# Optimization experiments

Measured on AMD Instinct MI355X. Metric: run time of the kernel, lower is better.

The kernel has to match this reference:

```python
import jax, jax.numpy as jnp
import numpy as np

NEG = 0.01
NEG2 = 0.2
EPS = 1e-5
K = 10            # args.nk // 2
B, N, NZ = 8, 2048, 128


def lrelu(x, s):
    return jnp.where(x >= 0, x, s * x)


def conv1(x, W, b):  # 1x1 Conv1d: x [B,C,N], W [O,C]
    return jnp.einsum('bcn,oc->bon', x, W) + b[None, :, None]


def conv2(x, W, b):  # 1x1 Conv2d: x [B,C,N,K], W [O,C]
    return jnp.einsum('bcnk,oc->bonk', x, W) + b[None, :, None, None]


def bn2d(x, g, b):  # BatchNorm2d, training-mode batch stats (torch default)
    m = jnp.mean(x, axis=(0, 2, 3), keepdims=True)
    v = jnp.var(x, axis=(0, 2, 3), keepdims=True)
    return g[None, :, None, None] * (x - m) * jax.lax.rsqrt(v + EPS) + b[None, :, None, None]


def edge_feats(x, k):
    # x [B,C,N] -> [B,2C,N,k]: cat(central, neighbor - central) over k-NN (self excluded)
    xt = jnp.swapaxes(x, 1, 2)                                   # [B,N,C]
    sq = jnp.sum(xt * xt, axis=-1)                               # [B,N]
    dist = sq[:, :, None] + sq[:, None, :] - 2.0 * jnp.einsum('bnc,bmc->bnm', xt, xt)
    idx = jnp.argsort(dist, axis=2)[:, :, 1:k + 1]               # [B,N,k]
    nb = jax.vmap(lambda xb, ib: xb[:, ib])(x, idx)              # [B,C,N,k] gather
    central = jnp.broadcast_to(x[:, :, :, None], nb.shape)
    return jnp.concatenate([central, nb - central], axis=1)


def edge_block(x, Fin, w1, b1, g1, bb1, w2, b2, g2, bb2, xw, xb, xg, xbb, ow, ob):
    ee = edge_feats(x, K)                                        # [B,2Fin,N,K]
    w = lrelu(bn2d(conv2(ee[:, Fin:], w1, b1), g1, bb1), NEG)    # conv_w branch
    w = lrelu(bn2d(conv2(w, w2, b2), g2, bb2), NEG)
    w = jax.nn.softmax(w, axis=-1)                               # softmax over k neighbors
    h = lrelu(bn2d(conv2(ee, xw, xb), xg, xbb), NEG)             # conv_x branch
    h = h * w
    # conv_out: Conv2d(Fout, Fout, [1,K]) reduces k dim; ow [O,C,K]
    return jnp.einsum('bcnk,ock->bon', h, ow) + ob[None, :, None]


def _forward(x, z, head_w1, head_b1, head_w2, head_b2,
             e1_w1, e1_b1, e1_g1, e1_bb1, e1_w2, e1_b2, e1_g2, e1_bb2,
             e1_xw, e1_xb, e1_xg, e1_xbb, e1_ow, e1_ob,
             ad1_w, ad1_b, lat_w, lat_b,
             e2_w1, e2_b1, e2_g1, e2_bb1, e2_w2, e2_b2, e2_g2, e2_bb2,
             e2_xw, e2_xb, e2_xg, e2_xbb, e2_ow, e2_ob,
             ad2_w, ad2_b,
             tail_w1, tail_b1, tail_w2, tail_b2, tail_w3, tail_b3):
    style = lrelu(conv1(jnp.concatenate([x, z], axis=1), head_w1, head_b1), NEG)
    style = lrelu(conv1(style, head_w2, head_b2), NEG)           # [B,512,N]
    x1 = edge_block(x, 3, e1_w1, e1_b1, e1_g1, e1_bb1, e1_w2, e1_b2, e1_g2, e1_bb2,
                    e1_xw, e1_xb, e1_xg, e1_xbb, e1_ow, e1_ob)   # [B,128,N]
    x1 = lrelu(x1, NEG2)
    ga, be = jnp.split(conv1(style, ad1_w, ad1_b), 2, axis=1)    # AdaIN1
    x1 = ga * x1 + be                                            # NOTE: overwritten below (faithful to source)
    x1 = conv1(style, lat_w, lat_b)                              # conv_latent overwrites x1
    x2 = edge_block(x1, 128, e2_w1, e2_b1, e2_g1, e2_bb1, e2_w2, e2_b2, e2_g2, e2_bb2,
                    e2_xw, e2_xb, e2_xg, e2_xbb, e2_ow, e2_ob)   # [B,512,N]
    x2 = lrelu(x2, NEG2)
    ga2, be2 = jnp.split(conv1(style, ad2_w, ad2_b), 2, axis=1)  # AdaIN2
    x2 = ga2 * x2 + be2
    t = lrelu(conv1(x2, tail_w1, tail_b1), NEG)
    t = lrelu(conv1(t, tail_w2, tail_b2), NEG)
    return jnp.tanh(conv1(t, tail_w3, tail_b3))                  # [B,3,N]


def setup_inputs() -> dict:
    ks = iter(jax.random.split(jax.random.key(0), 80))
    def rnd(*shape):
        return jax.random.normal(next(ks), shape, jnp.float32) * 0.05
    z0 = lambda n: jnp.zeros((n,), jnp.float32)
    o1 = lambda n: jnp.ones((n,), jnp.float32)
    return dict(
        x=jax.random.normal(next(ks), (B, 3, N), jnp.float32),
        z=jax.random.normal(next(ks), (B, NZ, N), jnp.float32),
        head_w1=rnd(512, 3 + NZ), head_b1=z0(512),
        head_w2=rnd(512, 512), head_b2=z0(512),
        e1_w1=rnd(64, 3), e1_b1=z0(64), e1_g1=o1(64), e1_bb1=z0(64),
        e1_w2=rnd(128, 64), e1_b2=z0(128), e1_g2=o1(128), e1_bb2=z0(128),
        e1_xw=rnd(128, 6), e1_xb=z0(128), e1_xg=o1(128), e1_xbb=z0(128),
        e1_ow=rnd(128, 128, K), e1_ob=z0(128),
        ad1_w=rnd(256, 512), ad1_b=jnp.concatenate([o1(128), z0(128)]),
        lat_w=rnd(128, 512), lat_b=z0(128),
        e2_w1=rnd(256, 128), e2_b1=z0(256), e2_g1=o1(256), e2_bb1=z0(256),
        e2_w2=rnd(512, 256), e2_b2=z0(512), e2_g2=o1(512), e2_bb2=z0(512),
        e2_xw=rnd(512, 256), e2_xb=z0(512), e2_xg=o1(512), e2_xbb=z0(512),
        e2_ow=rnd(512, 512, K), e2_ob=z0(512),
        ad2_w=rnd(1024, 512), ad2_b=jnp.concatenate([o1(512), z0(512)]),
        tail_w1=rnd(256, 512), tail_b1=z0(256),
        tail_w2=rnd(64, 256), tail_b2=z0(64),
        tail_w3=rnd(3, 64), tail_b3=z0(3),
    )


def reference(x, z, head_w1, head_b1, head_w2, head_b2,
              e1_w1, e1_b1, e1_g1, e1_bb1, e1_w2, e1_b2, e1_g2, e1_bb2,
              e1_xw, e1_xb, e1_xg, e1_xbb, e1_ow, e1_ob,
              ad1_w, ad1_b, lat_w, lat_b,
              e2_w1, e2_b1, e2_g1, e2_bb1, e2_w2, e2_b2, e2_g2, e2_bb2,
              e2_xw, e2_xb, e2_xg, e2_xbb, e2_ow, e2_ob,
              ad2_w, ad2_b,
              tail_w1, tail_b1, tail_w2, tail_b2, tail_w3, tail_b3):
    return _forward(x, z, head_w1, head_b1, head_w2, head_b2,
                    e1_w1, e1_b1, e1_g1, e1_bb1, e1_w2, e1_b2, e1_g2, e1_bb2,
                    e1_xw, e1_xb, e1_xg, e1_xbb, e1_ow, e1_ob,
                    ad1_w, ad1_b, lat_w, lat_b,
                    e2_w1, e2_b1, e2_g1, e2_bb1, e2_w2, e2_b2, e2_g2, e2_bb2,
                    e2_xw, e2_xb, e2_xg, e2_xbb, e2_ow, e2_ob,
                    ad2_w, ad2_b,
                    tail_w1, tail_b1, tail_w2, tail_b2, tail_w3, tail_b3)
```

## Files before the change

### kernel.cpp

```cpp
#include <hip/hip_runtime.h>
#include <hip/hip_bf16.h>


using bf16 = __hip_bfloat16;
typedef short bf8_t __attribute__((ext_vector_type(8)));
typedef float f4_t __attribute__((ext_vector_type(4)));

#define DEV static __device__ __forceinline__
DEV void stf(float* p, float v) { *p = v; }
DEV void stf(bf16* p, float v) { *p = __float2bfloat16(v); }
DEV unsigned short f2b(float f) { bf16 h = __float2bfloat16(f); return *reinterpret_cast<unsigned short*>(&h); }
DEV float b2f(unsigned short u) { bf16 h; *reinterpret_cast<unsigned short*>(&h) = u; return __bfloat162float(h); }
DEV unsigned short ldb(const float* p) { return f2b(*p); }
DEV unsigned short ldb(const unsigned short* p) { return *p; }

template<int OMODE, int SPLITK, int ACT, typename TB, typename TO>
__global__ __launch_bounds__(256) void mfma_k(
    const unsigned short* __restrict__ Wb, const TB* __restrict__ X,
    const float* __restrict__ bias, TO* __restrict__ Out,
    int O, int K, int N, int kLen, long sXz, long sOz,
    double* __restrict__ gsum, double* __restrict__ gsq)
{
  int kOff = 0;
  if constexpr (SPLITK) { kOff = blockIdx.z * kLen; }
  else { X += (long)blockIdx.z * sXz; }
  int n0 = blockIdx.x * 128, o0 = blockIdx.y * 128;
  __shared__ unsigned short As[128][40];
  __shared__ unsigned short Bs[128][40];
  __shared__ float ssum[128], ssq[128];
  int t = threadIdx.x;
  int w = t >> 6, l = t & 63;
  int lr = l & 15, lk = l >> 4;
  f4_t acc[2][8];
#pragma unroll
  for (int mi = 0; mi < 2; ++mi)
#pragma unroll
    for (int nj = 0; nj < 8; ++nj) acc[mi][nj] = (f4_t){0.f, 0.f, 0.f, 0.f};

  for (int k0 = kOff; k0 < kOff + kLen; k0 += 32) {
    {
      int ro = t >> 3, kq = (t & 7) * 4;
#pragma unroll
      for (int i = 0; i < 4; ++i) {
        int o = ro + i * 32;
        unsigned long long v = *reinterpret_cast<const unsigned long long*>(
            &Wb[(long)(o0 + o) * K + k0 + kq]);
        *reinterpret_cast<unsigned long long*>(&As[o][kq]) = v;
      }
    }
    {
      int nn = t & 127, kb = (t >> 7) * 2;
#pragma unroll
      for (int i = 0; i < 8; ++i) {
        int kk = kb + i * 4;
        unsigned short b0 = ldb(&X[(long)(k0 + kk) * N + n0 + nn]);
        unsigned short b1 = ldb(&X[(long)(k0 + kk + 1) * N + n0 + nn]);
        *reinterpret_cast<unsigned int*>(&Bs[nn][kk]) =
            (unsigned)b0 | ((unsigned)b1 << 16);
      }
    }
    __syncthreads();
    bf8_t a[2], b[8];
#pragma unroll
    for (int mi = 0; mi < 2; ++mi)
      a[mi] = *reinterpret_cast<const bf8_t*>(&As[w * 32 + mi * 16 + lr][lk * 8]);
#pragma unroll
    for (int nj = 0; nj < 8; ++nj)
      b[nj] = *reinterpret_cast<const bf8_t*>(&Bs[nj * 16 + lr][lk * 8]);
#pragma unroll
    for (int mi = 0; mi < 2; ++mi)
#pragma unroll
      for (int nj = 0; nj < 8; ++nj)
        acc[mi][nj] = __builtin_amdgcn_mfma_f32_16x16x32_bf16(
            a[mi], b[nj], acc[mi][nj], 0, 0, 0);
    __syncthreads();
  }
  if constexpr (OMODE >= 1) {
    if (t < 128) { ssum[t] = 0.f; ssq[t] = 0.f; }
    __syncthreads();
#pragma unroll
    for (int mi = 0; mi < 2; ++mi)
#pragma unroll
      for (int jj = 0; jj < 4; ++jj) {
        float s = 0.f, s2 = 0.f;
#pragma unroll
        for (int nj = 0; nj < 8; ++nj) {
          float v = acc[mi][nj][jj];
          s += v; s2 = fmaf(v, v, s2);
        }
#pragma unroll
        for (int off = 1; off < 16; off <<= 1) {
          s += __shfl_xor(s, off);
          s2 += __shfl_xor(s2, off);
        }
        if (lr == 0) {
          int oi = w * 32 + mi * 16 + lk * 4 + jj;
          atomicAdd(&ssum[oi], s);
          atomicAdd(&ssq[oi], s2);
        }
      }
    __syncthreads();
    if (t < 128) {
      atomicAdd(&gsum[o0 + t], (double)ssum[t]);
      atomicAdd(&gsq[o0 + t], (double)ssq[t]);
    }
  }
  if constexpr (OMODE != 1) {
    TO* Ob = Out + (long)blockIdx.z * sOz;
#pragma unroll
    for (int mi = 0; mi < 2; ++mi)
#pragma unroll
      for (int nj = 0; nj < 8; ++nj)
#pragma unroll
        for (int jj = 0; jj < 4; ++jj) {
          int o = o0 + w * 32 + mi * 16 + lk * 4 + jj;
          int n = n0 + nj * 16 + lr;
          float v = acc[mi][nj][jj] + (bias ? bias[o] : 0.f);
          if constexpr (ACT == 1) v = v >= 0.f ? v : 0.01f * v;
          stf(&Ob[(long)o * N + n], v);
        }
  }
}

template<int ACT>
__global__ __launch_bounds__(256) void gemm2_k(
    const float* __restrict__ W, const float* __restrict__ X,
    const float* __restrict__ bias, float* __restrict__ Out,
    int O, int K, int N, int kLen, long sXz, long sOz)
{
  X += (long)blockIdx.z * sXz;
  int n0 = blockIdx.x * 128, o0 = blockIdx.y * 128;
  __shared__ float Ws[8][132];
  __shared__ float Xs[8][132];
  int t = threadIdx.x, tx = t & 15, ty = t >> 4;
  int cb = tx * 4;
  float acc[8][8] = {};
  for (int k0 = 0; k0 < kLen; k0 += 8) {
    {
      int kk = t & 7, oo0 = t >> 3;
#pragma unroll
      for (int i = 0; i < 4; ++i) {
        int oo = oo0 + i * 32;
        Ws[kk][oo] = W[(long)(o0 + oo) * K + k0 + kk];
      }
    }
    {
      int nn = t & 127, kk0 = t >> 7;
#pragma unroll
      for (int i = 0; i < 4; ++i) {
        int kk = kk0 + i * 2;
        Xs[kk][nn] = X[(long)(k0 + kk) * N + n0 + nn];
      }
    }
    __syncthreads();
#pragma unroll
    for (int kk = 0; kk < 8; ++kk) {
      float a[8], bx[8];
#pragma unroll
      for (int i = 0; i < 8; ++i) a[i] = Ws[kk][ty * 8 + i];
#pragma unroll
      for (int j = 0; j < 4; ++j) { bx[j] = Xs[kk][cb + j]; bx[4 + j] = Xs[kk][64 + cb + j]; }
#pragma unroll
      for (int i = 0; i < 8; ++i)
#pragma unroll
        for (int j = 0; j < 8; ++j)
          acc[i][j] = fmaf(a[i], bx[j], acc[i][j]);
    }
    __syncthreads();
  }
  float* Ob = Out + (long)blockIdx.z * sOz;
#pragma unroll
  for (int i = 0; i < 8; ++i) {
    int o = o0 + ty * 8 + i;
    float bv = bias ? bias[o] : 0.f;
#pragma unroll
    for (int j = 0; j < 8; ++j) {
      int col = (j < 4) ? (n0 + cb + j) : (n0 + 64 + cb + (j - 4));
      float v = acc[i][j] + bv;
      if constexpr (ACT == 1) v = v >= 0.f ? v : 0.01f * v;
      Ob[(long)o * N + col] = v;
    }
  }
}

__global__ __launch_bounds__(256) void gramg_k(const float* __restrict__ A,
                                               const float* __restrict__ sqb,
                                               float* __restrict__ D) {
  int m0 = blockIdx.x * 128, n0 = blockIdx.y * 128;
  __shared__ float Am[8][132];
  __shared__ float An[8][132];
  int t = threadIdx.x, tx = t & 15, ty = t >> 4;
  int cb = tx * 4;
  float g[8][8] = {};
  for (int c0 = 0; c0 < 128; c0 += 8) {
    {
      int nn = t & 127, kk0 = t >> 7;
#pragma unroll
      for (int i = 0; i < 4; ++i) {
        int kk = kk0 + i * 2;
        Am[kk][nn] = A[(long)(c0 + kk) * 2048 + m0 + nn];
        An[kk][nn] = A[(long)(c0 + kk) * 2048 + n0 + nn];
      }
    }
    __syncthreads();
#pragma unroll
    for (int kk = 0; kk < 8; ++kk) {
      float a[8], bm[8];
#pragma unroll
      for (int i = 0; i < 8; ++i) a[i] = An[kk][ty * 8 + i];
#pragma unroll
      for (int j = 0; j < 4; ++j) { bm[j] = Am[kk][cb + j]; bm[4 + j] = Am[kk][64 + cb + j]; }
#pragma unroll
      for (int i = 0; i < 8; ++i)
#pragma unroll
        for (int j = 0; j < 8; ++j)
          g[i][j] = fmaf(a[i], bm[j], g[i][j]);
    }
    __syncthreads();
  }
#pragma unroll
  for (int i = 0; i < 8; ++i) {
    int n = n0 + ty * 8 + i;
    float sn = sqb[n];
#pragma unroll
    for (int j = 0; j < 8; ++j) {
      int m = (j < 4) ? (m0 + cb + j) : (m0 + 64 + cb + (j - 4));
      float t1 = __fadd_rn(sn, sqb[m]);
      D[(long)n * 2048 + m] = __fsub_rn(t1, __fmul_rn(2.0f, g[i][j]));
    }
  }
}

__global__ void sqnp_k(const float* __restrict__ x1, float* __restrict__ sq) {
  int n = blockIdx.x * 256 + threadIdx.x;
  int b = blockIdx.y;
  const float* p = x1 + (long)b * 128 * 2048 + n;
  float r[4][16];
#pragma unroll
  for (int v = 0; v < 4; ++v)
#pragma unroll
    for (int l = 0; l < 16; ++l) {
      float x = p[(long)(16 * v + l) * 2048];
      r[v][l] = __fmul_rn(x, x);
    }
#pragma unroll
  for (int v = 0; v < 4; ++v)
#pragma unroll
    for (int l = 0; l < 16; ++l) {
      float x = p[(long)(64 + 16 * v + l) * 2048];
      r[v][l] = __fadd_rn(r[v][l], __fmul_rn(x, x));
    }
  float u[16];
#pragma unroll
  for (int l = 0; l < 16; ++l)
    u[l] = __fadd_rn(__fadd_rn(r[0][l], r[1][l]), __fadd_rn(r[2][l], r[3][l]));
  float b8[8];
#pragma unroll
  for (int l = 0; l < 8; ++l) b8[l] = __fadd_rn(u[l], u[l + 8]);
  float c4[4];
#pragma unroll
  for (int l = 0; l < 4; ++l) c4[l] = __fadd_rn(b8[l], b8[l + 4]);
  float d0 = __fadd_rn(c4[0], c4[2]);
  float d1 = __fadd_rn(c4[1], c4[3]);
  sq[b * 2048 + n] = __fadd_rn(d0, d1);
}

template<int ACT>
__global__ __launch_bounds__(256) void gemm_k(
    const float* __restrict__ W, const float* __restrict__ X,
    const float* __restrict__ bias, float* __restrict__ Out,
    int O, int K, int N, long sXb, long sOb, float slope)
{
  const float* Xb = X + (long)blockIdx.z * sXb;
  int n0 = blockIdx.x * 64, o0 = blockIdx.y * 64;
  __shared__ float Ws[16][68];
  __shared__ float Xs[16][68];
  int t = threadIdx.x, tx = t & 15, ty = t >> 4;
  float acc[16] = {};
  for (int k0 = 0; k0 < K; k0 += 16) {
#pragma unroll
    for (int i = 0; i < 4; ++i) {
      int l = t + i * 256, oo = l >> 4, kk = l & 15;
      int o = o0 + oo, k = k0 + kk;
      float v = 0.f;
      if (o < O && k < K) v = W[(long)o * K + k];
      Ws[kk][oo] = v;
    }
#pragma unroll
    for (int i = 0; i < 4; ++i) {
      int kk = (t >> 6) + i * 4, nn = t & 63;
      int k = k0 + kk;
      float v = 0.f;
      if (k < K) v = Xb[(long)k * N + n0 + nn];
      Xs[kk][nn] = v;
    }
    __syncthreads();
#pragma unroll
    for (int kk = 0; kk < 16; ++kk) {
      float a0 = Ws[kk][ty * 4 + 0], a1 = Ws[kk][ty * 4 + 1];
      float a2 = Ws[kk][ty * 4 + 2], a3 = Ws[kk][ty * 4 + 3];
      float b0 = Xs[kk][tx * 4 + 0], b1 = Xs[kk][tx * 4 + 1];
      float b2 = Xs[kk][tx * 4 + 2], b3 = Xs[kk][tx * 4 + 3];
      acc[0] = fmaf(a0, b0, acc[0]);   acc[1] = fmaf(a0, b1, acc[1]);
      acc[2] = fmaf(a0, b2, acc[2]);   acc[3] = fmaf(a0, b3, acc[3]);
      acc[4] = fmaf(a1, b0, acc[4]);   acc[5] = fmaf(a1, b1, acc[5]);
      acc[6] = fmaf(a1, b2, acc[6]);   acc[7] = fmaf(a1, b3, acc[7]);
      acc[8] = fmaf(a2, b0, acc[8]);   acc[9] = fmaf(a2, b1, acc[9]);
      acc[10] = fmaf(a2, b2, acc[10]); acc[11] = fmaf(a2, b3, acc[11]);
      acc[12] = fmaf(a3, b0, acc[12]); acc[13] = fmaf(a3, b1, acc[13]);
      acc[14] = fmaf(a3, b2, acc[14]); acc[15] = fmaf(a3, b3, acc[15]);
    }
    __syncthreads();
  }
#pragma unroll
  for (int i = 0; i < 4; ++i) {
    int o = o0 + ty * 4 + i;
    if (o < O) {
      float bv = bias ? bias[o] : 0.f;
#pragma unroll
      for (int j = 0; j < 4; ++j) {
        float v = acc[i * 4 + j] + bv;
        if constexpr (ACT == 1) v = v >= 0.f ? v : slope * v;
        if constexpr (ACT == 2) v = tanhf(v);
        Out[(long)blockIdx.z * sOb + (long)o * N + n0 + tx * 4 + j] = v;
      }
    }
  }
}

__global__ void fill_k(float* __restrict__ out, float v, int n) {
  int id = blockIdx.x * 256 + threadIdx.x;
  if (id < n) out[id] = v;
}

__global__ void wcvt_k(const float* __restrict__ in, unsigned short* __restrict__ o, long n) {
  long id = (long)blockIdx.x * 256 + threadIdx.x;
  if (id < n) o[id] = f2b(in[id]);
}

__global__ void wpad_k(const float* __restrict__ w, float* __restrict__ wp) {
  int id = blockIdx.x * 256 + threadIdx.x;
  if (id >= 512 * 136) return;
  int o = id / 136, k = id % 136;
  wp[id] = (k < 131) ? w[o * 131 + k] : 0.f;
}

__global__ void xz_k(const float* __restrict__ x, const float* __restrict__ z,
                     float* __restrict__ xz) {
  long id = (long)blockIdx.x * 256 + threadIdx.x;
  const long TOT = 8L * 136 * 2048;
  if (id >= TOT) return;
  int n = (int)(id % 2048);
  int c = (int)((id / 2048) % 136);
  int b = (int)(id / (136L * 2048));
  float v = 0.f;
  if (c < 3) v = x[((long)b * 3 + c) * 2048 + n];
  else if (c < 131) v = z[((long)b * 128 + (c - 3)) * 2048 + n];
  xz[id] = v;
}

__global__ void xwsplit_k(const float* __restrict__ xw,
                          unsigned short* __restrict__ Ab,
                          unsigned short* __restrict__ Bb) {
  int id = blockIdx.x * 256 + threadIdx.x;
  if (id >= 512 * 128) return;
  int o = id / 128, c = id % 128;
  float a = xw[o * 256 + c];
  float b = xw[o * 256 + 128 + c];
  Ab[id] = f2b(a - b);
  Bb[id] = f2b(b);
}

__global__ __launch_bounds__(256) void topk_k(const float* __restrict__ dist,
                                              int* __restrict__ idx) {
  int row = blockIdx.x * 4 + (threadIdx.x >> 6);
  int lane = threadIdx.x & 63;
  const float* rp = dist + (long)row * 2048;
  float v[32];
#pragma unroll
  for (int i = 0; i < 32; ++i) v[i] = rp[i * 64 + lane];
  unsigned taken = 0;
  const float INF = __builtin_inff();
  for (int r = 0; r < 11; ++r) {
    float best = INF; int bi = 0x7fffffff;
#pragma unroll
    for (int i = 0; i < 32; ++i) {
      bool free = !((taken >> i) & 1u);
      if (free && v[i] < best) { best = v[i]; bi = i; }
    }
    int gi = (bi == 0x7fffffff) ? 0x7ffffffe : bi * 64 + lane;
#pragma unroll
    for (int off = 32; off; off >>= 1) {
      float ov = __shfl_xor(best, off);
      int og = __shfl_xor(gi, off);
      if (ov < best || (ov == best && og < gi)) { best = ov; gi = og; }
    }
    if (gi >= 0 && gi < 2048) {
      if (lane == 0 && r > 0) idx[row * 10 + (r - 1)] = gi;
      if ((gi & 63) == lane) taken |= 1u << (gi >> 6);
    } else if (lane == 0 && r > 0) {
      idx[row * 10 + (r - 1)] = row;
    }
  }
}

__global__ void g_k(const float* __restrict__ Q, const int* __restrict__ idx,
                    const float* __restrict__ sc, const float* __restrict__ sh,
                    unsigned short* __restrict__ G) {
  long id = (long)blockIdx.x * 256 + threadIdx.x;
  const long TOT = 256L * 20480;
  if (id >= TOT) return;
  int m = (int)(id % 20480);
  int c = (int)(id / 20480);
  int j = idx[m];
  int n = m / 10;
  const float* Qc = Q + (long)c * 2048;
  float v = fmaf(sc[c], Qc[j] - Qc[n], sh[c]);
  v = v >= 0.f ? v : 0.01f * v;
  G[id] = f2b(v);
}

__global__ void redk_k(const float* __restrict__ P, const float* __restrict__ bias,
                       float* __restrict__ xo) {
  int id = blockIdx.x * 256 + threadIdx.x;
  if (id >= 512 * 2048) return;
  int o = id >> 11;
  float s = 0.f;
#pragma unroll
  for (int sp = 0; sp < 8; ++sp) s += P[(long)sp * 512 * 2048 + id];
  s += bias[o];
  xo[id] = s >= 0.f ? s : 0.2f * s;
}

__global__ __launch_bounds__(256) void stats_qd_k(const float* __restrict__ Q,
                                                  const int* __restrict__ idx,
                                                  double* __restrict__ sum,
                                                  double* __restrict__ sumsq) {
  int c = blockIdx.x, b = blockIdx.y;
  const float* Qp = Q + ((long)b * 256 + c) * 2048;
  const int* ip = idx + (long)b * 20480;
  __shared__ float Qs[2048];
  for (int i = threadIdx.x; i < 2048; i += 256) Qs[i] = Qp[i];
  __syncthreads();
  float s = 0.f, s2 = 0.f;
  for (int m = threadIdx.x; m < 20480; m += 256) {
    float v = Qs[ip[m]] - Qs[m / 10];
    s += v; s2 = fmaf(v, v, s2);
  }
  __shared__ float ls[256], ls2[256];
  ls[threadIdx.x] = s; ls2[threadIdx.x] = s2;
  __syncthreads();
  for (int st = 128; st > 0; st >>= 1) {
    if (threadIdx.x < st) { ls[threadIdx.x] += ls[threadIdx.x + st]; ls2[threadIdx.x] += ls2[threadIdx.x + st]; }
    __syncthreads();
  }
  if (threadIdx.x == 0) { atomicAdd(&sum[c], (double)ls[0]); atomicAdd(&sumsq[c], (double)ls2[0]); }
}

__global__ __launch_bounds__(256) void stats_cx_k(const float* __restrict__ R,
                                                  const float* __restrict__ S,
                                                  const int* __restrict__ idx,
                                                  double* __restrict__ sum,
                                                  double* __restrict__ sumsq) {
  int c = blockIdx.x, b = blockIdx.y;
  const float* Rp = R + ((long)b * 512 + c) * 2048;
  const float* Sp = S + ((long)b * 512 + c) * 2048;
  const int* ip = idx + (long)b * 20480;
  __shared__ float Rs[2048], Ss[2048];
  for (int i = threadIdx.x; i < 2048; i += 256) { Rs[i] = Rp[i]; Ss[i] = Sp[i]; }
  __syncthreads();
  float s = 0.f, s2 = 0.f;
  for (int m = threadIdx.x; m < 20480; m += 256) {
    float v = Rs[m / 10] + Ss[ip[m]];
    s += v; s2 = fmaf(v, v, s2);
  }
  __shared__ float ls[256], ls2[256];
  ls[threadIdx.x] = s; ls2[threadIdx.x] = s2;
  __syncthreads();
  for (int st = 128; st > 0; st >>= 1) {
    if (threadIdx.x < st) { ls[threadIdx.x] += ls[threadIdx.x + st]; ls2[threadIdx.x] += ls2[threadIdx.x + st]; }
    __syncthreads();
  }
  if (threadIdx.x == 0) { atomicAdd(&sum[c], (double)ls[0]); atomicAdd(&sumsq[c], (double)ls2[0]); }
}

__global__ void bnfin_k(const double* __restrict__ sum, const double* __restrict__ sumsq,
                        const float* __restrict__ g, const float* __restrict__ bb,
                        float* __restrict__ sc, float* __restrict__ sh, int C, double invcnt) {
  int c = blockIdx.x * 256 + threadIdx.x;
  if (c >= C) return;
  double mean = sum[c] * invcnt;
  double var = sumsq[c] * invcnt - mean * mean;
  float rstd = (float)(1.0 / sqrt(var + 1e-5));
  float scv = g[c] * rstd;
  sc[c] = scv;
  sh[c] = bb[c] - (float)mean * scv;
}

__global__ __launch_bounds__(256) void smxe_k(
    const bf16* __restrict__ wl, const float* __restrict__ sc2,
    const float* __restrict__ sh2, const float* __restrict__ R,
    const float* __restrict__ S, const int* __restrict__ ip,
    const float* __restrict__ sc3, const float* __restrict__ sh3,
    unsigned short* __restrict__ Xe) {
  int c = blockIdx.x;
  __shared__ float Ss[2048];
  const float* Sp = S + (long)c * 2048;
  const float* Rp = R + (long)c * 2048;
  for (int i = threadIdx.x; i < 2048; i += 256) Ss[i] = Sp[i];
  __syncthreads();
  float a = sc2[c], bs = sh2[c], a3 = sc3[c], b3 = sh3[c];
  const bf16* wc = wl + (long)c * 20480;
  for (int n = threadIdx.x; n < 2048; n += 256) {
    float v[10], m = -1e30f;
#pragma unroll
    for (int k = 0; k < 10; ++k) {
      float x = fmaf(a, __bfloat162float(wc[n * 10 + k]), bs);
      x = x >= 0.f ? x : 0.01f * x;
      v[k] = x; m = fmaxf(m, x);
    }
    float s = 0.f;
#pragma unroll
    for (int k = 0; k < 10; ++k) { v[k] = __expf(v[k] - m); s += v[k]; }
    float inv = 1.f / s;
    float rn = Rp[n];
#pragma unroll
    for (int k = 0; k < 10; ++k) {
      int j = ip[n * 10 + k];
      float h = fmaf(a3, rn + Ss[j], b3);
      h = h >= 0.f ? h : 0.01f * h;
      Xe[(long)(c * 10 + k) * 2048 + n] = f2b(h * (v[k] * inv));
    }
  }
}

__global__ void adain_k(float* __restrict__ x2, const float* __restrict__ ad2,
                        unsigned short* __restrict__ x2b) {
  long id = (long)blockIdx.x * 256 + threadIdx.x;
  const long TOT = 8L * 512 * 2048;
  if (id >= TOT) return;
  int n = (int)(id & 2047);
  long t = id >> 11;
  int c = (int)(t & 511);
  int b = (int)(t >> 9);
  const float* A = ad2 + (long)b * 1024 * 2048;
  float ga = A[(long)c * 2048 + n];
  float be = A[(long)(512 + c) * 2048 + n];
  float v = fmaf(ga, x2[id], be);
  x2[id] = v;
  x2b[id] = f2b(v);
}

extern "C" void kernel_launch(void* const* d_in, const int* in_sizes, int n_in,
                              void* d_out, int out_size, void* d_ws, size_t ws_size,
                              hipStream_t stream) {
  (void)in_sizes; (void)n_in;
  const float* xin     = (const float*)d_in[0];
  const float* zin     = (const float*)d_in[1];
  const float* head_w1 = (const float*)d_in[2];
  const float* head_b1 = (const float*)d_in[3];
  const float* head_w2 = (const float*)d_in[4];
  const float* head_b2 = (const float*)d_in[5];
  const float* lat_w   = (const float*)d_in[22];
  const float* lat_b   = (const float*)d_in[23];
  const float* e2_w1   = (const float*)d_in[24];
  const float* e2_g1   = (const float*)d_in[26];
  const float* e2_bb1  = (const float*)d_in[27];
  const float* e2_w2   = (const float*)d_in[28];
  const float* e2_g2   = (const float*)d_in[30];
  const float* e2_bb2  = (const float*)d_in[31];
  const float* e2_xw   = (const float*)d_in[32];
  const float* e2_xg   = (const float*)d_in[34];
  const float* e2_xbb  = (const float*)d_in[35];
  const float* e2_ow   = (const float*)d_in[36];
  const float* e2_ob   = (const float*)d_in[37];
  const float* ad2_w   = (const float*)d_in[38];
  const float* ad2_b   = (const float*)d_in[39];
  const float* tail_w1 = (const float*)d_in[40];
  const float* tail_b1 = (const float*)d_in[41];
  const float* tail_w2 = (const float*)d_in[42];
  const float* tail_b2 = (const float*)d_in[43];
  const float* tail_w3 = (const float*)d_in[44];
  const float* tail_b3 = (const float*)d_in[45];
  float* out = (float*)d_out;

  char* ws = (char*)d_ws;
  size_t off = 0;
  auto A = [&](size_t bytes) { size_t r = off; off += (bytes + 255) & ~(size_t)255; return r; };
  size_t oStats = A(20480);
  size_t oSc1 = A(1024), oSh1 = A(1024);
  size_t oSc2 = A(2048), oSh2 = A(2048);
  size_t oSc3 = A(2048), oSh3 = A(2048);
  size_t oXwAb = A(512 * 128 * 2), oXwBb = A(512 * 128 * 2);
  size_t oWp  = A(512 * 136 * 4);
  size_t oW2b = A(512 * 256 * 2);
  size_t oOwb = A(512L * 5120 * 2);
  size_t oAdb = A(1024 * 512 * 2);
  size_t oTw1b = A(256 * 512 * 2);
  size_t oSq  = A(8L * 2048 * 4);
  size_t oIdx = A(8L * 2048 * 10 * 4);
  size_t oX1  = A(8L * 128 * 2048 * 4);
  size_t oQ   = A(8L * 256 * 2048 * 4);
  size_t oR   = A(8L * 512 * 2048 * 4);
  size_t oS   = A(8L * 512 * 2048 * 4);
  size_t oStyle = A(8L * 512 * 2048 * 4);
  size_t oX2  = A(8L * 512 * 2048 * 4);
  size_t oSL  = A(83886080 + 512);
  size_t offBase = off;
  size_t oW2all = A(8L * 512 * 20480 * 2);
  size_t offFull = off;
  if (ws_size < offBase) {
    fill_k<<<(out_size + 255) / 256, 256, 0, stream>>>(out, (float)(ws_size >> 20), out_size);
    return;
  }
  bool pathA = ws_size >= offFull;

  double* sum1 = (double*)(ws + oStats);
  double* sumsq1 = sum1 + 256;
  double* sum2 = sumsq1 + 256;
  double* sumsq2 = sum2 + 512;
  double* sum3 = sumsq2 + 512;
  double* sumsq3 = sum3 + 512;
  float* sc1 = (float*)(ws + oSc1); float* sh1 = (float*)(ws + oSh1);
  float* sc2 = (float*)(ws + oSc2); float* sh2 = (float*)(ws + oSh2);
  float* sc3 = (float*)(ws + oSc3); float* sh3 = (float*)(ws + oSh3);
  unsigned short* xwAb = (unsigned short*)(ws + oXwAb);
  unsigned short* xwBb = (unsigned short*)(ws + oXwBb);
  float* Wp = (float*)(ws + oWp);
  unsigned short* w2b = (unsigned short*)(ws + oW2b);
  unsigned short* owb = (unsigned short*)(ws + oOwb);
  unsigned short* adb = (unsigned short*)(ws + oAdb);
  unsigned short* tw1b = (unsigned short*)(ws + oTw1b);
  float* sq = (float*)(ws + oSq);
  int* idx = (int*)(ws + oIdx);
  float* x1 = (float*)(ws + oX1);
  float* Q = (float*)(ws + oQ);
  float* R = (float*)(ws + oR);
  float* S = (float*)(ws + oS);
  float* style = (float*)(ws + oStyle);
  float* style1 = (float*)(ws + oX2);
  float* x2 = (float*)(ws + oX2);
  char* SL = ws + oSL;
  float* xzp = (float*)(SL);
  float* dist = (float*)(SL);
  unsigned short* x1b = (unsigned short*)(SL + 17825792);
  unsigned short* G = (unsigned short*)(SL);
  bf16* w2lb = (bf16*)(SL + 46137344);
  unsigned short* Xeb = (unsigned short*)(SL);
  float* P = (float*)(SL + 46137344);
  float* ad2out = (float*)(SL);
  unsigned short* x2b = (unsigned short*)(SL + 70254592);
  float* t1 = (float*)(SL);
  float* t2 = (float*)(SL + 20971520);
  bf16* w2all = (bf16*)(ws + oW2all);

  hipMemsetAsync(ws + oStats, 0, 20480, stream);

  wcvt_k<<<(512 * 256 + 255) / 256, 256, 0, stream>>>(e2_w2, w2b, 512 * 256);
  wcvt_k<<<(int)((512L * 5120 + 255) / 256), 256, 0, stream>>>(e2_ow, owb, 512L * 5120);
  wcvt_k<<<(1024 * 512 + 255) / 256, 256, 0, stream>>>(ad2_w, adb, 1024 * 512);
  wcvt_k<<<(256 * 512 + 255) / 256, 256, 0, stream>>>(tail_w1, tw1b, 256 * 512);

  wpad_k<<<(512 * 136 + 255) / 256, 256, 0, stream>>>(head_w1, Wp);
  xz_k<<<(8L * 136 * 2048 + 255) / 256, 256, 0, stream>>>(xin, zin, xzp);
  gemm2_k<1><<<dim3(16, 4, 8), 256, 0, stream>>>(
      Wp, xzp, head_b1, style1, 512, 136, 2048, 136, 136L * 2048, 512L * 2048);
  gemm2_k<1><<<dim3(16, 4, 8), 256, 0, stream>>>(
      head_w2, style1, head_b2, style, 512, 512, 2048, 512, 512L * 2048, 512L * 2048);
  gemm2_k<0><<<dim3(16, 1, 8), 256, 0, stream>>>(
      lat_w, style, lat_b, x1, 128, 512, 2048, 512, 512L * 2048, 128L * 2048);

  wcvt_k<<<(int)((8L * 128 * 2048 + 255) / 256), 256, 0, stream>>>(x1, x1b, 8L * 128 * 2048);

  sqnp_k<<<dim3(8, 8), 256, 0, stream>>>(x1, sq);
  for (int b = 0; b < 8; ++b) {
    gramg_k<<<dim3(16, 16), 256, 0, stream>>>(
        x1 + (long)b * 128 * 2048, sq + b * 2048, dist);
    topk_k<<<512, 256, 0, stream>>>(dist, idx + (long)b * 20480);
  }

  gemm_k<0><<<dim3(32, 4, 8), 256, 0, stream>>>(
      e2_w1, x1, nullptr, Q, 256, 128, 2048, 128L * 2048, 256L * 2048, 0.f);
  stats_qd_k<<<dim3(256, 8), 256, 0, stream>>>(Q, idx, sum1, sumsq1);
  bnfin_k<<<1, 256, 0, stream>>>(sum1, sumsq1, e2_g1, e2_bb1, sc1, sh1, 256, 1.0 / 163840.0);

  xwsplit_k<<<(512 * 128 + 255) / 256, 256, 0, stream>>>(e2_xw, xwAb, xwBb);
  mfma_k<0, 0, 0, unsigned short, float><<<dim3(16, 4, 8), 256, 0, stream>>>(
      xwAb, x1b, nullptr, R, 512, 128, 2048, 128, 128L * 2048, 512L * 2048,
      nullptr, nullptr);
  mfma_k<0, 0, 0, unsigned short, float><<<dim3(16, 4, 8), 256, 0, stream>>>(
      xwBb, x1b, nullptr, S, 512, 128, 2048, 128, 128L * 2048, 512L * 2048,
      nullptr, nullptr);
  stats_cx_k<<<dim3(512, 8), 256, 0, stream>>>(R, S, idx, sum3, sumsq3);
  bnfin_k<<<2, 256, 0, stream>>>(sum3, sumsq3, e2_xg, e2_xbb, sc3, sh3, 512, 1.0 / 163840.0);

  if (pathA) {
    for (int b = 0; b < 8; ++b) {
      g_k<<<20480, 256, 0, stream>>>(Q + (long)b * 256 * 2048, idx + (long)b * 20480,
                                     sc1, sh1, G);
      mfma_k<2, 0, 0, unsigned short, bf16><<<dim3(160, 4, 1), 256, 0, stream>>>(
          w2b, G, nullptr, w2all + (long)b * 512 * 20480, 512, 256, 20480, 256,
          0, 0, sum2, sumsq2);
    }
    bnfin_k<<<2, 256, 0, stream>>>(sum2, sumsq2, e2_g2, e2_bb2, sc2, sh2, 512, 1.0 / 163840.0);
    for (int b = 0; b < 8; ++b) {
      smxe_k<<<512, 256, 0, stream>>>(
          w2all + (long)b * 512 * 20480, sc2, sh2,
          R + (long)b * 512 * 2048, S + (long)b * 512 * 2048,
          idx + (long)b * 20480, sc3, sh3, Xeb);
      mfma_k<0, 1, 0, unsigned short, float><<<dim3(16, 4, 8), 256, 0, stream>>>(
          owb, Xeb, nullptr, P, 512, 5120, 2048, 640, 0, 512L * 2048,
          nullptr, nullptr);
      redk_k<<<(512 * 2048 + 255) / 256, 256, 0, stream>>>(
          P, e2_ob, x2 + (long)b * 512 * 2048);
    }
  } else {
    for (int b = 0; b < 8; ++b) {
      g_k<<<20480, 256, 0, stream>>>(Q + (long)b * 256 * 2048, idx + (long)b * 20480,
                                     sc1, sh1, G);
      mfma_k<1, 0, 0, unsigned short, float><<<dim3(160, 4, 1), 256, 0, stream>>>(
          w2b, G, nullptr, nullptr, 512, 256, 20480, 256, 0, 0, sum2, sumsq2);
    }
    bnfin_k<<<2, 256, 0, stream>>>(sum2, sumsq2, e2_g2, e2_bb2, sc2, sh2, 512, 1.0 / 163840.0);
    for (int b = 0; b < 8; ++b) {
      g_k<<<20480, 256, 0, stream>>>(Q + (long)b * 256 * 2048, idx + (long)b * 20480,
                                     sc1, sh1, G);
      mfma_k<0, 0, 0, unsigned short, bf16><<<dim3(160, 4, 1), 256, 0, stream>>>(
          w2b, G, nullptr, w2lb, 512, 256, 20480, 256, 0, 0, nullptr, nullptr);
      smxe_k<<<512, 256, 0, stream>>>(
          w2lb, sc2, sh2,
          R + (long)b * 512 * 2048, S + (long)b * 512 * 2048,
          idx + (long)b * 20480, sc3, sh3, Xeb);
      mfma_k<0, 1, 0, unsigned short, float><<<dim3(16, 4, 8), 256, 0, stream>>>(
          owb, Xeb, nullptr, P, 512, 5120, 2048, 640, 0, 512L * 2048,
          nullptr, nullptr);
      redk_k<<<(512 * 2048 + 255) / 256, 256, 0, stream>>>(
          P, e2_ob, x2 + (long)b * 512 * 2048);
    }
  }

  mfma_k<0, 0, 0, float, float><<<dim3(16, 8, 8), 256, 0, stream>>>(
      adb, style, ad2_b, ad2out, 1024, 512, 2048, 512, 512L * 2048, 1024L * 2048,
      nullptr, nullptr);
  adain_k<<<(8L * 512 * 2048 + 255) / 256, 256, 0, stream>>>(x2, ad2out, x2b);

  mfma_k<0, 0, 1, unsigned short, float><<<dim3(16, 2, 8), 256, 0, stream>>>(
      tw1b, x2b, tail_b1, t1, 256, 512, 2048, 512, 512L * 2048, 256L * 2048,
      nullptr, nullptr);
  gemm_k<1><<<dim3(32, 1, 8), 256, 0, stream>>>(
      tail_w2, t1, tail_b2, t2, 64, 256, 2048, 256L * 2048, 64L * 2048, 0.01f);
  gemm_k<2><<<dim3(32, 1, 8), 256, 0, stream>>>(
      tail_w3, t2, tail_b3, out, 3, 64, 2048, 64L * 2048, 3L * 2048, 0.f);
}
```

Before: 1.896 ms.

## Batch edge-block kernels over batch pairs and vectorize bf16 B-tile loads

Processes two batch items per launch for the gram/top-k stage, the G-construction plus stats GEMM, and the conv_out split-K GEMM with its reduction. This gives larger grids and fewer launches. The mfma kernel gains a hybrid split-K mode that combines a batch offset with a 4-way K split. The bf16 B-tile loader now reads two columns per 32-bit load. The large w2all path is removed, so the second GEMM pass is always recomputed, and the workspace layout is reshuffled to hold the paired buffers.

After: 1.622 ms. 1.17x faster.

```diff
diff --git a/kernel.cpp b/kernel.cpp
--- a/kernel.cpp
+++ b/kernel.cpp
@@ -10,7 +10,6 @@
 DEV void stf(float* p, float v) { *p = v; }
 DEV void stf(bf16* p, float v) { *p = __float2bfloat16(v); }
 DEV unsigned short f2b(float f) { bf16 h = __float2bfloat16(f); return *reinterpret_cast<unsigned short*>(&h); }
-DEV float b2f(unsigned short u) { bf16 h; *reinterpret_cast<unsigned short*>(&h) = u; return __bfloat162float(h); }
 DEV unsigned short ldb(const float* p) { return f2b(*p); }
 DEV unsigned short ldb(const unsigned short* p) { return *p; }
 
@@ -22,7 +21,8 @@
     double* __restrict__ gsum, double* __restrict__ gsq)
 {
   int kOff = 0;
-  if constexpr (SPLITK) { kOff = blockIdx.z * kLen; }
+  if constexpr (SPLITK == 1) { kOff = blockIdx.z * kLen; }
+  else if constexpr (SPLITK == 2) { kOff = (blockIdx.z & 3) * kLen; X += (long)(blockIdx.z >> 2) * sXz; }
   else { X += (long)blockIdx.z * sXz; }
   int n0 = blockIdx.x * 128, o0 = blockIdx.y * 128;
   __shared__ unsigned short As[128][40];
@@ -48,7 +48,17 @@
         *reinterpret_cast<unsigned long long*>(&As[o][kq]) = v;
       }
     }
-    {
+    if constexpr (sizeof(TB) == 2) {
+      int nn = (t & 63) * 2, kg = (t >> 6) * 8;
+#pragma unroll
+      for (int i = 0; i < 8; ++i) {
+        int kk = kg + i;
+        unsigned v = *reinterpret_cast<const unsigned*>(
+            &X[(long)(k0 + kk) * N + n0 + nn]);
+        Bs[nn][kk] = (unsigned short)(v & 0xffffu);
+        Bs[nn + 1][kk] = (unsigned short)(v >> 16);
+      }
+    } else {
       int nn = t & 127, kb = (t >> 7) * 2;
 #pragma unroll
       for (int i = 0; i < 8; ++i) {
@@ -75,7 +85,7 @@
             a[mi], b[nj], acc[mi][nj], 0, 0, 0);
     __syncthreads();
   }
-  if constexpr (OMODE >= 1) {
+  if constexpr (OMODE == 1) {
     if (t < 128) { ssum[t] = 0.f; ssq[t] = 0.f; }
     __syncthreads();
 #pragma unroll
@@ -104,8 +114,7 @@
       atomicAdd(&gsum[o0 + t], (double)ssum[t]);
       atomicAdd(&gsq[o0 + t], (double)ssq[t]);
     }
-  }
-  if constexpr (OMODE != 1) {
+  } else {
     TO* Ob = Out + (long)blockIdx.z * sOz;
 #pragma unroll
     for (int mi = 0; mi < 2; ++mi)
@@ -186,6 +195,9 @@
 __global__ __launch_bounds__(256) void gramg_k(const float* __restrict__ A,
                                                const float* __restrict__ sqb,
                                                float* __restrict__ D) {
+  A += (long)blockIdx.z * 128 * 2048;
+  sqb += (long)blockIdx.z * 2048;
+  D += (long)blockIdx.z * 2048 * 2048;
   int m0 = blockIdx.x * 128, n0 = blockIdx.y * 128;
   __shared__ float Am[8][132];
   __shared__ float An[8][132];
@@ -399,37 +411,41 @@
       if (lane == 0 && r > 0) idx[row * 10 + (r - 1)] = gi;
       if ((gi & 63) == lane) taken |= 1u << (gi >> 6);
     } else if (lane == 0 && r > 0) {
-      idx[row * 10 + (r - 1)] = row;
-    }
-  }
-}
-
-__global__ void g_k(const float* __restrict__ Q, const int* __restrict__ idx,
-                    const float* __restrict__ sc, const float* __restrict__ sh,
-                    unsigned short* __restrict__ G) {
+      idx[row * 10 + (r - 1)] = row & 2047;
+    }
+  }
+}
+
+__global__ void g2_k(const float* __restrict__ Q, const int* __restrict__ idx,
+                     const float* __restrict__ sc, const float* __restrict__ sh,
+                     unsigned short* __restrict__ G, int nb) {
   long id = (long)blockIdx.x * 256 + threadIdx.x;
-  const long TOT = 256L * 20480;
-  if (id >= TOT) return;
-  int m = (int)(id % 20480);
-  int c = (int)(id / 20480);
-  int j = idx[m];
+  const long per = 256L * 20480;
+  if (id >= (long)nb * per) return;
+  int b = (int)(id / per);
+  long r = id % per;
+  int c = (int)(r / 20480);
+  int m = (int)(r % 20480);
+  int j = idx[(long)b * 20480 + m];
   int n = m / 10;
-  const float* Qc = Q + (long)c * 2048;
+  const float* Qc = Q + (long)b * 256 * 2048 + (long)c * 2048;
   float v = fmaf(sc[c], Qc[j] - Qc[n], sh[c]);
   v = v >= 0.f ? v : 0.01f * v;
   G[id] = f2b(v);
 }
 
-__global__ void redk_k(const float* __restrict__ P, const float* __restrict__ bias,
-                       float* __restrict__ xo) {
+__global__ void redk2_k(const float* __restrict__ P, const float* __restrict__ bias,
+                        float* __restrict__ xo) {
   int id = blockIdx.x * 256 + threadIdx.x;
-  if (id >= 512 * 2048) return;
-  int o = id >> 11;
+  if (id >= 2 * 512 * 2048) return;
+  int bi = id / (512 * 2048);
+  int r = id % (512 * 2048);
+  int o = r >> 11;
   float s = 0.f;
 #pragma unroll
-  for (int sp = 0; sp < 8; ++sp) s += P[(long)sp * 512 * 2048 + id];
+  for (int sp = 0; sp < 4; ++sp) s += P[(long)(bi * 4 + sp) * 512 * 2048 + r];
   s += bias[o];
-  xo[id] = s >= 0.f ? s : 0.2f * s;
+  xo[(long)bi * 512 * 2048 + r] = s >= 0.f ? s : 0.2f * s;
 }
 
 __global__ __launch_bounds__(256) void stats_qd_k(const float* __restrict__ Q,
@@ -607,13 +623,10 @@
   size_t oX2  = A(8L * 512 * 2048 * 4);
   size_t oSL  = A(83886080 + 512);
   size_t offBase = off;
-  size_t oW2all = A(8L * 512 * 20480 * 2);
-  size_t offFull = off;
   if (ws_size < offBase) {
     fill_k<<<(out_size + 255) / 256, 256, 0, stream>>>(out, (float)(ws_size >> 20), out_size);
     return;
   }
-  bool pathA = ws_size >= offFull;
 
   double* sum1 = (double*)(ws + oStats);
   double* sumsq1 = sum1 + 256;
@@ -642,17 +655,17 @@
   float* x2 = (float*)(ws + oX2);
   char* SL = ws + oSL;
   float* xzp = (float*)(SL);
-  float* dist = (float*)(SL);
-  unsigned short* x1b = (unsigned short*)(SL + 17825792);
-  unsigned short* G = (unsigned short*)(SL);
+  unsigned short* x1b = (unsigned short*)(SL + 41943040);
+  float* dist2 = (float*)(SL);
+  unsigned short* G2 = (unsigned short*)(SL);
+  unsigned short* Xe2 = (unsigned short*)(SL);
   bf16* w2lb = (bf16*)(SL + 46137344);
-  unsigned short* Xeb = (unsigned short*)(SL);
+  unsigned short* G1 = (unsigned short*)(SL + 69206016);
   float* P = (float*)(SL + 46137344);
   float* ad2out = (float*)(SL);
   unsigned short* x2b = (unsigned short*)(SL + 70254592);
   float* t1 = (float*)(SL);
   float* t2 = (float*)(SL + 20971520);
-  bf16* w2all = (bf16*)(ws + oW2all);
 
   hipMemsetAsync(ws + oStats, 0, 20480, stream);
 
@@ -673,10 +686,10 @@
   wcvt_k<<<(int)((8L * 128 * 2048 + 255) / 256), 256, 0, stream>>>(x1, x1b, 8L * 128 * 2048);
 
   sqnp_k<<<dim3(8, 8), 256, 0, stream>>>(x1, sq);
-  for (int b = 0; b < 8; ++b) {
-    gramg_k<<<dim3(16, 16), 256, 0, stream>>>(
-        x1 + (long)b * 128 * 2048, sq + b * 2048, dist);
-    topk_k<<<512, 256, 0, stream>>>(dist, idx + (long)b * 20480);
+  for (int bp = 0; bp < 8; bp += 2) {
+    gramg_k<<<dim3(16, 16, 2), 256, 0, stream>>>(
+        x1 + (long)bp * 128 * 2048, sq + bp * 2048, dist2);
+    topk_k<<<1024, 256, 0, stream>>>(dist2, idx + (long)bp * 20480);
   }
 
   gemm_k<0><<<dim3(32, 4, 8), 256, 0, stream>>>(
@@ -694,55 +707,37 @@
   stats_cx_k<<<dim3(512, 8), 256, 0, stream>>>(R, S, idx, sum3, sumsq3);
   bnfin_k<<<2, 256, 0, stream>>>(sum3, sumsq3, e2_xg, e2_xbb, sc3, sh3, 512, 1.0 / 163840.0);
 
-  if (pathA) {
-    for (int b = 0; b < 8; ++b) {
-      g_k<<<20480, 256, 0, stream>>>(Q + (long)b * 256 * 2048, idx + (long)b * 20480,
-                                     sc1, sh1, G);
-      mfma_k<2, 0, 0, unsigned short, bf16><<<dim3(160, 4, 1), 256, 0, stream>>>(
-          w2b, G, nullptr, w2all + (long)b * 512 * 20480, 512, 256, 20480, 256,
-          0, 0, sum2, sumsq2);
-    }
-    bnfin_k<<<2, 256, 0, stream>>>(sum2, sumsq2, e2_g2, e2_bb2, sc2, sh2, 512, 1.0 / 163840.0);
-    for (int b = 0; b < 8; ++b) {
+  for (int bp = 0; bp < 8; bp += 2) {
+    g2_k<<<2 * 20480, 256, 0, stream>>>(Q + (long)bp * 256 * 2048,
+                                        idx + (long)bp * 20480, sc1, sh1, G2, 2);
+    mfma_k<1, 0, 0, unsigned short, float><<<dim3(160, 4, 2), 256, 0, stream>>>(
+        w2b, G2, nullptr, nullptr, 512, 256, 20480, 256, 256L * 20480, 0,
+        sum2, sumsq2);
+  }
+  bnfin_k<<<2, 256, 0, stream>>>(sum2, sumsq2, e2_g2, e2_bb2, sc2, sh2, 512, 1.0 / 163840.0);
+
+  for (int bp = 0; bp < 8; bp += 2) {
+    for (int bi = 0; bi < 2; ++bi) {
+      int b = bp + bi;
+      g2_k<<<20480, 256, 0, stream>>>(Q + (long)b * 256 * 2048,
+                                      idx + (long)b * 20480, sc1, sh1, G1, 1);
+      mfma_k<0, 0, 0, unsigned short, bf16><<<dim3(160, 4, 1), 256, 0, stream>>>(
+          w2b, G1, nullptr, w2lb, 512, 256, 20480, 256, 0, 0, nullptr, nullptr);
       smxe_k<<<512, 256, 0, stream>>>(
-          w2all + (long)b * 512 * 20480, sc2, sh2,
-          R + (long)b * 512 * 2048, S + (long)b * 512 * 2048,
-          idx + (long)b * 20480, sc3, sh3, Xeb);
-      mfma_k<0, 1, 0, unsigned short, float><<<dim3(16, 4, 8), 256, 0, stream>>>(
-          owb, Xeb, nullptr, P, 512, 5120, 2048, 640, 0, 512L * 2048,
-          nullptr, nullptr);
-      redk_k<<<(512 * 2048 + 255) / 256, 256, 0, stream>>>(
-          P, e2_ob, x2 + (long)b * 512 * 2048);
-    }
-  } else {
-    for (int b = 0; b < 8; ++b) {
-      g_k<<<20480, 256, 0, stream>>>(Q + (long)b * 256 * 2048, idx + (long)b * 20480,
-                                     sc1, sh1, G);
-      mfma_k<1, 0, 0, unsigned short, float><<<dim3(160, 4, 1), 256, 0, stream>>>(
-          w2b, G, nullptr, nullptr, 512, 256, 20480, 256, 0, 0, sum2, sumsq2);
-    }
-    bnfin_k<<<2, 256, 0, stream>>>(sum2, sumsq2, e2_g2, e2_bb2, sc2, sh2, 512, 1.0 / 163840.0);
-    for (int b = 0; b < 8; ++b) {
-      g_k<<<20480, 256, 0, stream>>>(Q + (long)b * 256 * 2048, idx + (long)b * 20480,
-                                     sc1, sh1, G);
-      mfma_k<0, 0, 0, unsigned short, bf16><<<dim3(160, 4, 1), 256, 0, stream>>>(
-          w2b, G, nullptr, w2lb, 512, 256, 20480, 256, 0, 0, nullptr, nullptr);
-      smxe_k<<<512, 256, 0, stream>>>(
-          w2lb, sc2, sh2,
-          R + (long)b * 512 * 2048, S + (long)b * 512 * 2048,
-          idx + (long)b * 20480, sc3, sh3, Xeb);
-      mfma_k<0, 1, 0, unsigned short, float><<<dim3(16, 4, 8), 256, 0, stream>>>(
-          owb, Xeb, nullptr, P, 512, 5120, 2048, 640, 0, 512L * 2048,
-          nullptr, nullptr);
-      redk_k<<<(512 * 2048 + 255) / 256, 256, 0, stream>>>(
-          P, e2_ob, x2 + (long)b * 512 * 2048);
-    }
+          w2lb, sc2, sh2, R + (long)b * 512 * 2048, S + (long)b * 512 * 2048,
+          idx + (long)b * 20480, sc3, sh3, Xe2 + (long)bi * 5120 * 2048);
+    }
+    mfma_k<0, 2, 0, unsigned short, float><<<dim3(16, 4, 8), 256, 0, stream>>>(
+        owb, Xe2, nullptr, P, 512, 5120, 2048, 1280, 5120L * 2048, 512L * 2048,
+        nullptr, nullptr);
+    redk2_k<<<(2 * 512 * 2048 + 255) / 256, 256, 0, stream>>>(
+        P, e2_ob, x2 + (long)bp * 512 * 2048);
   }
 
   mfma_k<0, 0, 0, float, float><<<dim3(16, 8, 8), 256, 0, stream>>>(
       adb, style, ad2_b, ad2out, 1024, 512, 2048, 512, 512L * 2048, 1024L * 2048,
       nullptr, nullptr);
-  adain_k<<<(8L * 512 * 2048 + 255) / 256, 256, 0, stream>>>(x2, ad2out, x2b);
+  adain_k<<<(int)((8L * 512 * 2048 + 255) / 256), 256, 0, stream>>>(x2, ad2out, x2b);
 
   mfma_k<0, 0, 1, unsigned short, float><<<dim3(16, 2, 8), 256, 0, stream>>>(
       tw1b, x2b, tail_b1, t1, 256, 512, 2048, 512, 512L * 2048, 256L * 2048,
```
